# Kernel tuning notes

Hardware: AMD Instinct MI355X
Metric: run time of the kernel (lower is better)

The kernel has to match this reference:

```python
import math
import jax, jax.numpy as jnp
import numpy as np

B, T, C = 8, 4096, 1024
N_HEAD = 16
HS = C // N_HEAD  # head_size = 64


def _keep_indices(T):
    # Faithful Python/math replication of the row-gather index list.
    a = math.ceil(T / 4)
    keep = [T - 1 - x for x in range(a)]
    keep += [T - 1 - math.ceil(3 / a * (x - a) ** 2 + a) for x in range(a, math.ceil(T / 2))]
    return np.array(list(reversed(keep)), dtype=np.int32)  # [K] = [ceil(T/2)]


def setup_inputs() -> dict:
    key = jax.random.key(0)
    ks = jax.random.split(key, 7)
    s = 1.0 / math.sqrt(C)  # torch Linear default init scale
    return {
        "x": jax.random.normal(ks[0], (B, T, C), dtype=jnp.float32),
        "Wq": jax.random.uniform(ks[1], (HS, C), jnp.float32, -s, s),
        "bq": jax.random.uniform(ks[2], (HS,), jnp.float32, -s, s),
        "Wk": jax.random.uniform(ks[3], (HS, C), jnp.float32, -s, s),
        "bk": jax.random.uniform(ks[4], (HS,), jnp.float32, -s, s),
        "Wv": jax.random.uniform(ks[5], (HS, C), jnp.float32, -s, s),
        "bv": jax.random.uniform(ks[6], (HS,), jnp.float32, -s, s),
    }


def reference(x, Wq, bq, Wk, bk, Wv, bv):
    Bx, Tx, Cx = x.shape
    keep = jnp.asarray(_keep_indices(Tx))                    # [K], static
    q = x @ Wq.T + bq                                        # [B,T,hs]
    k = x @ Wk.T + bk                                        # [B,T,hs]
    v = x @ Wv.T + bv                                        # [B,T,hs]
    # Original computes full q@k^T then gathers rows; gathering q rows first
    # is the same math without materializing [B,T,T].
    qg = q[:, keep, :]                                       # [B,K,hs]
    att = jnp.einsum('bkd,btd->bkt', qg, k) * (Cx ** -0.5)   # scale by n_embd, per source
    # fade_tril = tril[keep, :T]: row i allows positions j <= keep[i]
    mask = jnp.arange(Tx)[None, :] <= keep[:, None]          # [K,T]
    att = jnp.where(mask[None], att, -jnp.inf)
    att = jax.nn.softmax(att, axis=-1)
    # dropout p=0.0 -> identity
    out = jnp.einsum('bkt,btd->bkd', att, v)                 # [B,K,hs]
    return out
```

## Files before the change

### kernel.cpp

```cpp
#include <hip/hip_runtime.h>
#include <hip/hip_bf16.h>

typedef __attribute__((ext_vector_type(8))) short s8v;
typedef __attribute__((ext_vector_type(4))) short s4v;
typedef __attribute__((ext_vector_type(4))) float f4v;

#define B_   8
#define T_   4096
#define C_   1024
#define HS_  64
#define K2_  2048

__device__ __forceinline__ int keep_of(int i) {
    if (i >= 1024) return 2048 + i;
    int d = 1023 - i;
    return 3071 - ((3 * d * d + 1023) >> 10);
}

__device__ __forceinline__ short bf16_bits(float f) {
    union { __hip_bfloat16 h; short s; } u;
    u.h = __float2bfloat16(f);
    return u.s;
}

__device__ __forceinline__ s8v cvt8f(const float* p) {
    const f4v a = *(const f4v*)p;
    const f4v b = *(const f4v*)(p + 4);
    s8v r;
    r[0] = bf16_bits(a[0]); r[1] = bf16_bits(a[1]);
    r[2] = bf16_bits(a[2]); r[3] = bf16_bits(a[3]);
    r[4] = bf16_bits(b[0]); r[5] = bf16_bits(b[1]);
    r[6] = bf16_bits(b[2]); r[7] = bf16_bits(b[3]);
    return r;
}

__device__ __forceinline__ void gload_lds16(const void* g, void* l) {
    __builtin_amdgcn_global_load_lds(
        (__attribute__((address_space(1))) void*)(g),
        (__attribute__((address_space(3))) void*)(l), 16, 0, 0);
}

__global__ __launch_bounds__(256) void wcvt_kernel(
    const float* __restrict__ Wq, const float* __restrict__ Wk,
    const float* __restrict__ Wv, short* __restrict__ Wb)
{
    const int idx = (blockIdx.x * 256 + threadIdx.x) * 8;
    const int mat = idx >> 16;
    const int off = idx & 65535;
    const float* src = (mat == 0) ? Wq : (mat == 1) ? Wk : Wv;
    *(s8v*)(Wb + idx) = cvt8f(src + off);
}

__global__ __launch_bounds__(256) void qkv_kernel(
    const float* __restrict__ x,
    const short* __restrict__ Wb,
    const float* __restrict__ bq, const float* __restrict__ bk,
    const float* __restrict__ bv,
    __hip_bfloat16* __restrict__ Qo, __hip_bfloat16* __restrict__ Ko,
    __hip_bfloat16* __restrict__ Vt)
{
    __shared__ __align__(16) char smem[40960];
    float* xs  = (float*)smem;
    short* wsm = (short*)(smem + 16384);

    const int tid  = threadIdx.x;
    const int wave = tid >> 6;
    const int lane = tid & 63;
    const int l16  = lane & 15;
    const int quad = lane >> 4;
    const int row0 = blockIdx.x * 64;

    f4v acc[3][4];
    #pragma unroll
    for (int m = 0; m < 3; ++m)
        #pragma unroll
        for (int mt = 0; mt < 4; ++mt) {
            acc[m][mt][0] = 0.f; acc[m][mt][1] = 0.f;
            acc[m][mt][2] = 0.f; acc[m][mt][3] = 0.f;
        }

    int xrow[4], xoff[4];
    #pragma unroll
    for (int i = 0; i < 4; ++i) {
        const int f = 256 * i + tid;
        xrow[i] = f >> 4;
        xoff[i] = ((f & 15) ^ (xrow[i] & 7)) * 4;
    }
    int wrow[6], woff[6];
    #pragma unroll
    for (int i = 0; i < 6; ++i) {
        const int f = 256 * i + tid;
        wrow[i] = f >> 3;
        woff[i] = ((f & 7) ^ (wrow[i] & 7)) * 8;
    }

    for (int k0 = 0; k0 < C_; k0 += 64) {
        __syncthreads();
        #pragma unroll
        for (int i = 0; i < 4; ++i)
            gload_lds16(x + (size_t)(row0 + xrow[i]) * C_ + k0 + xoff[i],
                        (char*)xs + (256 * i + tid) * 16);
        #pragma unroll
        for (int i = 0; i < 6; ++i)
            gload_lds16(Wb + (size_t)wrow[i] * C_ + k0 + woff[i],
                        (char*)wsm + (256 * i + tid) * 16);
        __syncthreads();

        #pragma unroll
        for (int kh = 0; kh < 2; ++kh) {
            s8v a[4];
            #pragma unroll
            for (int mt = 0; mt < 4; ++mt) {
                const int r   = mt * 16 + l16;
                const int ch0 = kh * 8 + quad * 2;
                const float* p0 = xs + r * 64 + ((ch0    ) ^ (r & 7)) * 4;
                const float* p1 = xs + r * 64 + ((ch0 + 1) ^ (r & 7)) * 4;
                const f4v u = *(const f4v*)p0;
                const f4v v = *(const f4v*)p1;
                s8v af;
                af[0] = bf16_bits(u[0]); af[1] = bf16_bits(u[1]);
                af[2] = bf16_bits(u[2]); af[3] = bf16_bits(u[3]);
                af[4] = bf16_bits(v[0]); af[5] = bf16_bits(v[1]);
                af[6] = bf16_bits(v[2]); af[7] = bf16_bits(v[3]);
                a[mt] = af;
            }
            #pragma unroll
            for (int m = 0; m < 3; ++m) {
                const int wr = m * 64 + wave * 16 + l16;
                const int ch = kh * 4 + quad;
                const s8v bf = *(const s8v*)(wsm + wr * 64 + ((ch ^ (wr & 7)) * 8));
                #pragma unroll
                for (int mt = 0; mt < 4; ++mt)
                    acc[m][mt] = __builtin_amdgcn_mfma_f32_16x16x32_bf16(a[mt], bf, acc[m][mt], 0, 0, 0);
            }
        }
    }

    const int wc = wave * 16 + l16;
    const float bqv = bq[wc], bkv = bk[wc], bvv = bv[wc];
    #pragma unroll
    for (int mt = 0; mt < 4; ++mt) {
        const int rbase = row0 + mt * 16 + quad * 4;
        #pragma unroll
        for (int r = 0; r < 4; ++r) {
            Qo[(size_t)(rbase + r) * HS_ + wc] = __float2bfloat16(acc[0][mt][r] + bqv);
            Ko[(size_t)(rbase + r) * HS_ + wc] = __float2bfloat16(acc[1][mt][r] + bkv);
        }
        s4v vp;
        #pragma unroll
        for (int r = 0; r < 4; ++r) vp[r] = bf16_bits(acc[2][mt][r] + bvv);
        const int bb = rbase >> 12;
        const int t  = rbase & (T_ - 1);
        *(s4v*)(Vt + (size_t)bb * HS_ * T_
                   + (size_t)(t & ~63) * HS_ + wc * 64 + (t & 63)) = vp;
    }
}

__global__ __launch_bounds__(256) void attn_kernel(
    const __hip_bfloat16* __restrict__ Qo,
    const __hip_bfloat16* __restrict__ Ko,
    const __hip_bfloat16* __restrict__ Vt,
    float* __restrict__ out)
{
    __shared__ __align__(16) char smem[73728];
    short* Ks = (short*)smem;
    short* Vs = (short*)(smem + 32768);
    float* mL = (float*)smem;
    float* mO = (float*)(smem + 256);

    const int b    = blockIdx.x & 7;
    const int pp   = blockIdx.x >> 3;
    const int tid  = threadIdx.x;
    const int wave = tid >> 6;
    const int lane = tid & 63;
    const int l16  = lane & 15;
    const int quad = lane >> 4;

    short* pw = (short*)(smem + 65536) + wave * 1024;

    const short* kb = (const short*)Ko + (size_t)b * T_ * HS_;
    const short* vb = (const short*)Vt + (size_t)b * HS_ * T_;

    int kgoff[8], vgoff[8];
    #pragma unroll
    for (int j = 0; j < 8; ++j) {
        const int ki = j * 256 + tid;
        const int kr = ki >> 3;
        kgoff[j] = kr * 64 + (((tid & 7) ^ (kr & 7)) * 8);
        const int vs_ = ki >> 9;
        const int vd  = (ki & 511) >> 3;
        vgoff[j] = (vs_ * 64 + vd) * 64 + (((tid & 7) ^ (vd & 7)) * 8);
    }

    #pragma unroll 1
    for (int which = 0; which < 2; ++which) {
        const int qb = which ? (63 - pp) : (64 + pp);

        const int qt = keep_of(qb * 16 + l16);
        const __hip_bfloat16* qrow = Qo + ((size_t)(b * T_ + qt)) * HS_;
        const s8v aq0 = *(const s8v*)(qrow + quad * 8);
        const s8v aq1 = *(const s8v*)(qrow + 32 + quad * 8);

        int keepr[4];
        #pragma unroll
        for (int r = 0; r < 4; ++r) keepr[r] = keep_of(qb * 16 + quad * 4 + r);

        const int kmin   = keep_of(qb * 16);
        const int tmax   = keep_of(qb * 16 + 15);
        const int ntiles = (tmax >> 6) + 1;
        const int nsteps = (ntiles + 3) >> 2;

        f4v accO[4];
        #pragma unroll
        for (int j = 0; j < 4; ++j) { accO[j][0]=0.f; accO[j][1]=0.f; accO[j][2]=0.f; accO[j][3]=0.f; }
        float l_p[4] = {0.f, 0.f, 0.f, 0.f};

        for (int s = 0; s < nsteps; ++s) {
            const int t064 = s << 14;

            __syncthreads();
            #pragma unroll
            for (int j = 0; j < 8; ++j)
                gload_lds16(kb + t064 + kgoff[j], (char*)smem + (j * 256 + tid) * 16);
            #pragma unroll
            for (int j = 0; j < 8; ++j)
                gload_lds16(vb + t064 + vgoff[j], (char*)smem + 32768 + (j * 256 + tid) * 16);
            __syncthreads();

            const int ttg = s * 4 + wave;
            if (ttg < ntiles) {
                const int t0 = ttg << 6;

                f4v s4[4];
                #pragma unroll
                for (int jn = 0; jn < 4; ++jn) {
                    const int row = wave * 64 + jn * 16 + l16;
                    const s8v bk0 = *(const s8v*)(Ks + row * 64 + (((quad    ) ^ (row & 7)) * 8));
                    const s8v bk1 = *(const s8v*)(Ks + row * 64 + (((quad + 4) ^ (row & 7)) * 8));
                    f4v z; z[0]=0.f; z[1]=0.f; z[2]=0.f; z[3]=0.f;
                    z = __builtin_amdgcn_mfma_f32_16x16x32_bf16(aq0, bk0, z, 0, 0, 0);
                    z = __builtin_amdgcn_mfma_f32_16x16x32_bf16(aq1, bk1, z, 0, 0, 0);
                    s4[jn] = z;
                }

                if (t0 + 63 <= kmin) {
                    #pragma unroll
                    for (int jn = 0; jn < 4; ++jn) {
                        const int t = jn * 16 + l16;
                        const int chunk = t >> 3;
                        #pragma unroll
                        for (int r = 0; r < 4; ++r) {
                            const float p = __expf(s4[jn][r] * 0.03125f);
                            l_p[r] += p;
                            const int m = quad * 4 + r;
                            pw[m * 64 + ((chunk ^ (m & 7)) * 8) + (t & 7)] = bf16_bits(p);
                        }
                    }
                } else {
                    #pragma unroll
                    for (int jn = 0; jn < 4; ++jn) {
                        const int t = jn * 16 + l16;
                        const int valid_t = t0 + t;
                        const int chunk = t >> 3;
                        #pragma unroll
                        for (int r = 0; r < 4; ++r) {
                            const float e = __expf(s4[jn][r] * 0.03125f);
                            const float p = (valid_t <= keepr[r]) ? e : 0.0f;
                            l_p[r] += p;
                            const int m = quad * 4 + r;
                            pw[m * 64 + ((chunk ^ (m & 7)) * 8) + (t & 7)] = bf16_bits(p);
                        }
                    }
                }
                const s8v ap0 = *(const s8v*)(pw + l16 * 64 + ((quad    ) ^ (l16 & 7)) * 8);
                const s8v ap1 = *(const s8v*)(pw + l16 * 64 + ((quad + 4) ^ (l16 & 7)) * 8);

                #pragma unroll
                for (int jd = 0; jd < 4; ++jd) {
                    const int rd = jd * 16 + l16;
                    const s8v bv0 = *(const s8v*)(Vs + wave * 4096 + rd * 64 + (((quad    ) ^ (rd & 7)) * 8));
                    const s8v bv1 = *(const s8v*)(Vs + wave * 4096 + rd * 64 + (((quad + 4) ^ (rd & 7)) * 8));
                    accO[jd] = __builtin_amdgcn_mfma_f32_16x16x32_bf16(ap0, bv0, accO[jd], 0, 0, 0);
                    accO[jd] = __builtin_amdgcn_mfma_f32_16x16x32_bf16(ap1, bv1, accO[jd], 0, 0, 0);
                }
            }
        }

        #pragma unroll
        for (int off = 1; off < 16; off <<= 1)
            #pragma unroll
            for (int r = 0; r < 4; ++r) l_p[r] += __shfl_xor(l_p[r], off);

        __syncthreads();
        #pragma unroll
        for (int r = 0; r < 4; ++r) {
            const int row = quad * 4 + r;
            if (l16 == 0) mL[wave * 16 + row] = l_p[r];
            #pragma unroll
            for (int jd = 0; jd < 4; ++jd)
                mO[wave * 1024 + row * 64 + jd * 16 + l16] = accO[jd][r];
        }
        __syncthreads();

        {
            const int row = tid >> 4;
            const int col = (tid & 15) * 4;
            float L = 0.f;
            #pragma unroll
            for (int w = 0; w < 4; ++w) L += mL[w * 16 + row];
            const float inv = 1.0f / L;
            f4v o; o[0]=0.f; o[1]=0.f; o[2]=0.f; o[3]=0.f;
            #pragma unroll
            for (int w = 0; w < 4; ++w) {
                const f4v ow = *(const f4v*)(mO + w * 1024 + row * 64 + col);
                #pragma unroll
                for (int j = 0; j < 4; ++j) o[j] += ow[j];
            }
            #pragma unroll
            for (int j = 0; j < 4; ++j) o[j] *= inv;
            *(f4v*)(out + ((size_t)(b * K2_ + qb * 16 + row)) * HS_ + col) = o;
        }
        __syncthreads();
    }
}

extern "C" void kernel_launch(void* const* d_in, const int* in_sizes, int n_in,
                              void* d_out, int out_size, void* d_ws, size_t ws_size,
                              hipStream_t stream) {
    (void)in_sizes; (void)n_in; (void)out_size; (void)ws_size;
    const float* x  = (const float*)d_in[0];
    const float* Wq = (const float*)d_in[1];
    const float* bq = (const float*)d_in[2];
    const float* Wk = (const float*)d_in[3];
    const float* bk = (const float*)d_in[4];
    const float* Wv = (const float*)d_in[5];
    const float* bv = (const float*)d_in[6];

    __hip_bfloat16* Qo = (__hip_bfloat16*)d_ws;
    __hip_bfloat16* Ko = Qo + (size_t)B_ * T_ * HS_;
    __hip_bfloat16* Vt = Ko + (size_t)B_ * T_ * HS_;
    short*          Wb = (short*)(Vt + (size_t)B_ * HS_ * T_);
    float* o = (float*)d_out;

    wcvt_kernel<<<dim3(96), dim3(256), 0, stream>>>(Wq, Wk, Wv, Wb);
    qkv_kernel<<<dim3((B_ * T_) / 64), dim3(256), 0, stream>>>(
        x, Wb, bq, bk, bv, Qo, Ko, Vt);
    attn_kernel<<<dim3(512), dim3(256), 0, stream>>>(Qo, Ko, Vt, o);
}
```

Before: 252.6 us.

## Double-buffer LDS tiles in QKV projection and attention with finer key chunks

The QKV projection loop now double-buffers its x and weight tiles in shared memory, so loads for the next K slice are issued before the current slice is computed. The attention kernel also double-buffers its K/V tiles and shrinks each wave's key chunk from 64 to 32 positions. That cuts per-step staging and makes the causal tail finer-grained, while the next tile's load overlaps compute. The cost is double the LDS in the QKV kernel, which may reduce occupancy, plus more loop iterations with half as many MFMAs per step in attention.

```diff
diff --git a/kernel.cpp b/kernel.cpp
--- a/kernel.cpp
+++ b/kernel.cpp
@@ -59,9 +59,7 @@
     __hip_bfloat16* __restrict__ Qo, __hip_bfloat16* __restrict__ Ko,
     __hip_bfloat16* __restrict__ Vt)
 {
-    __shared__ __align__(16) char smem[40960];
-    float* xs  = (float*)smem;
-    short* wsm = (short*)(smem + 16384);
+    __shared__ __align__(16) char smem[81920];
 
     const int tid  = threadIdx.x;
     const int wave = tid >> 6;
@@ -94,17 +92,34 @@
         woff[i] = ((f & 7) ^ (wrow[i] & 7)) * 8;
     }
 
-    for (int k0 = 0; k0 < C_; k0 += 64) {
-        __syncthreads();
-        #pragma unroll
-        for (int i = 0; i < 4; ++i)
-            gload_lds16(x + (size_t)(row0 + xrow[i]) * C_ + k0 + xoff[i],
-                        (char*)xs + (256 * i + tid) * 16);
-        #pragma unroll
-        for (int i = 0; i < 6; ++i)
-            gload_lds16(Wb + (size_t)wrow[i] * C_ + k0 + woff[i],
-                        (char*)wsm + (256 * i + tid) * 16);
-        __syncthreads();
+    #pragma unroll
+    for (int i = 0; i < 4; ++i)
+        gload_lds16(x + (size_t)(row0 + xrow[i]) * C_ + xoff[i],
+                    (char*)smem + (256 * i + tid) * 16);
+    #pragma unroll
+    for (int i = 0; i < 6; ++i)
+        gload_lds16(Wb + (size_t)wrow[i] * C_ + woff[i],
+                    (char*)smem + 32768 + (256 * i + tid) * 16);
+    __syncthreads();
+
+    int buf = 0;
+    for (int ks = 0; ks < 16; ++ks) {
+        if (ks < 15) {
+            const int k0n = (ks + 1) * 64;
+            const int xb = (buf ^ 1) * 16384;
+            const int wb2 = (buf ^ 1) * 24576;
+            #pragma unroll
+            for (int i = 0; i < 4; ++i)
+                gload_lds16(x + (size_t)(row0 + xrow[i]) * C_ + k0n + xoff[i],
+                            (char*)smem + xb + (256 * i + tid) * 16);
+            #pragma unroll
+            for (int i = 0; i < 6; ++i)
+                gload_lds16(Wb + (size_t)wrow[i] * C_ + k0n + woff[i],
+                            (char*)smem + 32768 + wb2 + (256 * i + tid) * 16);
+        }
+
+        const float* xsc = (const float*)(smem + buf * 16384);
+        const short* wsc = (const short*)(smem + 32768 + buf * 24576);
 
         #pragma unroll
         for (int kh = 0; kh < 2; ++kh) {
@@ -113,8 +128,8 @@
             for (int mt = 0; mt < 4; ++mt) {
                 const int r   = mt * 16 + l16;
                 const int ch0 = kh * 8 + quad * 2;
-                const float* p0 = xs + r * 64 + ((ch0    ) ^ (r & 7)) * 4;
-                const float* p1 = xs + r * 64 + ((ch0 + 1) ^ (r & 7)) * 4;
+                const float* p0 = xsc + r * 64 + ((ch0    ) ^ (r & 7)) * 4;
+                const float* p1 = xsc + r * 64 + ((ch0 + 1) ^ (r & 7)) * 4;
                 const f4v u = *(const f4v*)p0;
                 const f4v v = *(const f4v*)p1;
                 s8v af;
@@ -128,12 +143,14 @@
             for (int m = 0; m < 3; ++m) {
                 const int wr = m * 64 + wave * 16 + l16;
                 const int ch = kh * 4 + quad;
-                const s8v bf = *(const s8v*)(wsm + wr * 64 + ((ch ^ (wr & 7)) * 8));
+                const s8v bf = *(const s8v*)(wsc + wr * 64 + ((ch ^ (wr & 7)) * 8));
                 #pragma unroll
                 for (int mt = 0; mt < 4; ++mt)
                     acc[m][mt] = __builtin_amdgcn_mfma_f32_16x16x32_bf16(a[mt], bf, acc[m][mt], 0, 0, 0);
             }
         }
+        __syncthreads();
+        buf ^= 1;
     }
 
     const int wc = wave * 16 + l16;
@@ -162,9 +179,9 @@
     const __hip_bfloat16* __restrict__ Vt,
     float* __restrict__ out)
 {
-    __shared__ __align__(16) char smem[73728];
-    short* Ks = (short*)smem;
-    short* Vs = (short*)(smem + 32768);
+    __shared__ __align__(16) char smem[69632];
+    short* Kb = (short*)smem;
+    short* Vb = (short*)(smem + 32768);
     float* mL = (float*)smem;
     float* mO = (float*)(smem + 256);
 
@@ -176,20 +193,20 @@
     const int l16  = lane & 15;
     const int quad = lane >> 4;
 
-    short* pw = (short*)(smem + 65536) + wave * 1024;
+    short* pw = (short*)(smem + 65536) + wave * 512;
 
     const short* kb = (const short*)Ko + (size_t)b * T_ * HS_;
     const short* vb = (const short*)Vt + (size_t)b * HS_ * T_;
 
-    int kgoff[8], vgoff[8];
-    #pragma unroll
-    for (int j = 0; j < 8; ++j) {
-        const int ki = j * 256 + tid;
-        const int kr = ki >> 3;
-        kgoff[j] = kr * 64 + (((tid & 7) ^ (kr & 7)) * 8);
-        const int vs_ = ki >> 9;
-        const int vd  = (ki & 511) >> 3;
-        vgoff[j] = (vs_ * 64 + vd) * 64 + (((tid & 7) ^ (vd & 7)) * 8);
+    int koff[4], voff[4];
+    #pragma unroll
+    for (int i = 0; i < 4; ++i) {
+        const int f = i * 256 + tid;
+        const int kr = f >> 3;
+        koff[i] = kr * 64 + (((f & 7) ^ (kr & 7)) * 8);
+        const int vt_ = f >> 9;
+        const int vd  = (f >> 3) & 63;
+        voff[i] = vt_ * 4096 + vd * 64 + (((f & 7) ^ (vd & 7)) * 8);
     }
 
     #pragma unroll 1
@@ -207,83 +224,96 @@
 
         const int kmin   = keep_of(qb * 16);
         const int tmax   = keep_of(qb * 16 + 15);
-        const int ntiles = (tmax >> 6) + 1;
-        const int nsteps = (ntiles + 3) >> 2;
+        const int nt32   = (tmax >> 5) + 1;
+        const int nsteps = (nt32 + 3) >> 2;
 
         f4v accO[4];
         #pragma unroll
         for (int j = 0; j < 4; ++j) { accO[j][0]=0.f; accO[j][1]=0.f; accO[j][2]=0.f; accO[j][3]=0.f; }
         float l_p[4] = {0.f, 0.f, 0.f, 0.f};
 
+        #pragma unroll
+        for (int i = 0; i < 4; ++i)
+            gload_lds16(kb + koff[i], (char*)smem + (i * 256 + tid) * 16);
+        #pragma unroll
+        for (int i = 0; i < 4; ++i)
+            gload_lds16(vb + voff[i], (char*)smem + 32768 + (i * 256 + tid) * 16);
+        __syncthreads();
+
+        int buf = 0;
         for (int s = 0; s < nsteps; ++s) {
-            const int t064 = s << 14;
-
-            __syncthreads();
-            #pragma unroll
-            for (int j = 0; j < 8; ++j)
-                gload_lds16(kb + t064 + kgoff[j], (char*)smem + (j * 256 + tid) * 16);
-            #pragma unroll
-            for (int j = 0; j < 8; ++j)
-                gload_lds16(vb + t064 + vgoff[j], (char*)smem + 32768 + (j * 256 + tid) * 16);
-            __syncthreads();
-
-            const int ttg = s * 4 + wave;
-            if (ttg < ntiles) {
-                const int t0 = ttg << 6;
-
-                f4v s4[4];
-                #pragma unroll
-                for (int jn = 0; jn < 4; ++jn) {
-                    const int row = wave * 64 + jn * 16 + l16;
-                    const s8v bk0 = *(const s8v*)(Ks + row * 64 + (((quad    ) ^ (row & 7)) * 8));
-                    const s8v bk1 = *(const s8v*)(Ks + row * 64 + (((quad + 4) ^ (row & 7)) * 8));
+            if (s + 1 < nsteps) {
+                const int goff = (s + 1) * 8192;
+                const int ldsb = (buf ^ 1) * 16384;
+                #pragma unroll
+                for (int i = 0; i < 4; ++i)
+                    gload_lds16(kb + goff + koff[i],
+                                (char*)smem + ldsb + (i * 256 + tid) * 16);
+                #pragma unroll
+                for (int i = 0; i < 4; ++i)
+                    gload_lds16(vb + goff + voff[i],
+                                (char*)smem + 32768 + ldsb + (i * 256 + tid) * 16);
+            }
+
+            const int c = s * 4 + wave;
+            if (c < nt32) {
+                const int t0 = c << 5;
+                const short* Kc = Kb + buf * 8192;
+                const short* Vc = Vb + buf * 8192 + (wave >> 1) * 4096;
+                const int tch = (wave & 1) * 4;
+
+                f4v s2[2];
+                #pragma unroll
+                for (int jn = 0; jn < 2; ++jn) {
+                    const int row = wave * 32 + jn * 16 + l16;
+                    const s8v bk0 = *(const s8v*)(Kc + row * 64 + (((quad    ) ^ (row & 7)) * 8));
+                    const s8v bk1 = *(const s8v*)(Kc + row * 64 + (((quad + 4) ^ (row & 7)) * 8));
                     f4v z; z[0]=0.f; z[1]=0.f; z[2]=0.f; z[3]=0.f;
                     z = __builtin_amdgcn_mfma_f32_16x16x32_bf16(aq0, bk0, z, 0, 0, 0);
                     z = __builtin_amdgcn_mfma_f32_16x16x32_bf16(aq1, bk1, z, 0, 0, 0);
-                    s4[jn] = z;
+                    s2[jn] = z;
                 }
 
-                if (t0 + 63 <= kmin) {
+                if (t0 + 31 <= kmin) {
                     #pragma unroll
-                    for (int jn = 0; jn < 4; ++jn) {
+                    for (int jn = 0; jn < 2; ++jn) {
                         const int t = jn * 16 + l16;
                         const int chunk = t >> 3;
                         #pragma unroll
                         for (int r = 0; r < 4; ++r) {
-                            const float p = __expf(s4[jn][r] * 0.03125f);
+                            const float p = __expf(s2[jn][r] * 0.03125f);
                             l_p[r] += p;
                             const int m = quad * 4 + r;
-                            pw[m * 64 + ((chunk ^ (m & 7)) * 8) + (t & 7)] = bf16_bits(p);
+                            pw[m * 32 + ((chunk ^ (m & 3)) * 8) + (t & 7)] = bf16_bits(p);
                         }
                     }
                 } else {
                     #pragma unroll
-                    for (int jn = 0; jn < 4; ++jn) {
+                    for (int jn = 0; jn < 2; ++jn) {
                         const int t = jn * 16 + l16;
                         const int valid_t = t0 + t;
                         const int chunk = t >> 3;
                         #pragma unroll
                         for (int r = 0; r < 4; ++r) {
-                            const float e = __expf(s4[jn][r] * 0.03125f);
+                            const float e = __expf(s2[jn][r] * 0.03125f);
                             const float p = (valid_t <= keepr[r]) ? e : 0.0f;
                             l_p[r] += p;
                             const int m = quad * 4 + r;
-                            pw[m * 64 + ((chunk ^ (m & 7)) * 8) + (t & 7)] = bf16_bits(p);
+                            pw[m * 32 + ((chunk ^ (m & 3)) * 8) + (t & 7)] = bf16_bits(p);
                         }
                     }
                 }
-                const s8v ap0 = *(const s8v*)(pw + l16 * 64 + ((quad    ) ^ (l16 & 7)) * 8);
-                const s8v ap1 = *(const s8v*)(pw + l16 * 64 + ((quad + 4) ^ (l16 & 7)) * 8);
+                const s8v ap = *(const s8v*)(pw + l16 * 32 + ((quad ^ (l16 & 3)) * 8));
 
                 #pragma unroll
                 for (int jd = 0; jd < 4; ++jd) {
                     const int rd = jd * 16 + l16;
-                    const s8v bv0 = *(const s8v*)(Vs + wave * 4096 + rd * 64 + (((quad    ) ^ (rd & 7)) * 8));
-                    const s8v bv1 = *(const s8v*)(Vs + wave * 4096 + rd * 64 + (((quad + 4) ^ (rd & 7)) * 8));
-                    accO[jd] = __builtin_amdgcn_mfma_f32_16x16x32_bf16(ap0, bv0, accO[jd], 0, 0, 0);
-                    accO[jd] = __builtin_amdgcn_mfma_f32_16x16x32_bf16(ap1, bv1, accO[jd], 0, 0, 0);
+                    const s8v bv = *(const s8v*)(Vc + rd * 64 + (((tch + quad) ^ (rd & 7)) * 8));
+                    accO[jd] = __builtin_amdgcn_mfma_f32_16x16x32_bf16(ap, bv, accO[jd], 0, 0, 0);
                 }
             }
+            __syncthreads();
+            buf ^= 1;
         }
 
         #pragma unroll
```

Result: slower. 260.5 us (+3.1%).

## Process both query blocks in one pass over shared K/V tiles

Applied to the files above, without the earlier changes.

Each block used to stream its K/V tiles twice, once for each of its two paired query blocks. Now both query blocks are processed against the same staged K/V tile in a single loop, and the K and V fragments are loaded from LDS into registers once and reused. Block-to-work mapping is also reversed so the heaviest blocks launch first. This halves the global-to-LDS loads and barriers but roughly doubles accumulator register pressure, which may lower occupancy.

```diff
diff --git a/kernel.cpp b/kernel.cpp
--- a/kernel.cpp
+++ b/kernel.cpp
@@ -169,7 +169,7 @@
     float* mO = (float*)(smem + 256);
 
     const int b    = blockIdx.x & 7;
-    const int pp   = blockIdx.x >> 3;
+    const int pp   = 63 - (blockIdx.x >> 3);
     const int tid  = threadIdx.x;
     const int wave = tid >> 6;
     const int lane = tid & 63;
@@ -192,58 +192,75 @@
         vgoff[j] = (vs_ * 64 + vd) * 64 + (((tid & 7) ^ (vd & 7)) * 8);
     }
 
-    #pragma unroll 1
-    for (int which = 0; which < 2; ++which) {
-        const int qb = which ? (63 - pp) : (64 + pp);
-
+    const int qbs[2] = { 64 + pp, 63 - pp };
+
+    s8v aq[2][2];
+    int keepr[2][4], kmin[2], ntl[2];
+    #pragma unroll
+    for (int e = 0; e < 2; ++e) {
+        const int qb = qbs[e];
         const int qt = keep_of(qb * 16 + l16);
         const __hip_bfloat16* qrow = Qo + ((size_t)(b * T_ + qt)) * HS_;
-        const s8v aq0 = *(const s8v*)(qrow + quad * 8);
-        const s8v aq1 = *(const s8v*)(qrow + 32 + quad * 8);
-
-        int keepr[4];
-        #pragma unroll
-        for (int r = 0; r < 4; ++r) keepr[r] = keep_of(qb * 16 + quad * 4 + r);
-
-        const int kmin   = keep_of(qb * 16);
-        const int tmax   = keep_of(qb * 16 + 15);
-        const int ntiles = (tmax >> 6) + 1;
-        const int nsteps = (ntiles + 3) >> 2;
-
-        f4v accO[4];
-        #pragma unroll
-        for (int j = 0; j < 4; ++j) { accO[j][0]=0.f; accO[j][1]=0.f; accO[j][2]=0.f; accO[j][3]=0.f; }
-        float l_p[4] = {0.f, 0.f, 0.f, 0.f};
-
-        for (int s = 0; s < nsteps; ++s) {
-            const int t064 = s << 14;
-
-            __syncthreads();
-            #pragma unroll
-            for (int j = 0; j < 8; ++j)
-                gload_lds16(kb + t064 + kgoff[j], (char*)smem + (j * 256 + tid) * 16);
-            #pragma unroll
-            for (int j = 0; j < 8; ++j)
-                gload_lds16(vb + t064 + vgoff[j], (char*)smem + 32768 + (j * 256 + tid) * 16);
-            __syncthreads();
-
-            const int ttg = s * 4 + wave;
-            if (ttg < ntiles) {
-                const int t0 = ttg << 6;
+        aq[e][0] = *(const s8v*)(qrow + quad * 8);
+        aq[e][1] = *(const s8v*)(qrow + 32 + quad * 8);
+        #pragma unroll
+        for (int r = 0; r < 4; ++r) keepr[e][r] = keep_of(qb * 16 + quad * 4 + r);
+        kmin[e] = keep_of(qb * 16);
+        ntl[e]  = (keep_of(qb * 16 + 15) >> 6) + 1;
+    }
+    const int nsteps = (ntl[0] + 3) >> 2;
+
+    f4v accO[2][4];
+    float l_p[2][4];
+    #pragma unroll
+    for (int e = 0; e < 2; ++e)
+        #pragma unroll
+        for (int j = 0; j < 4; ++j) {
+            accO[e][j][0]=0.f; accO[e][j][1]=0.f; accO[e][j][2]=0.f; accO[e][j][3]=0.f;
+            l_p[e][j] = 0.f;
+        }
+
+    for (int s = 0; s < nsteps; ++s) {
+        const int t064 = s << 14;
+
+        __syncthreads();
+        #pragma unroll
+        for (int j = 0; j < 8; ++j)
+            gload_lds16(kb + t064 + kgoff[j], (char*)smem + (j * 256 + tid) * 16);
+        #pragma unroll
+        for (int j = 0; j < 8; ++j)
+            gload_lds16(vb + t064 + vgoff[j], (char*)smem + 32768 + (j * 256 + tid) * 16);
+        __syncthreads();
+
+        const int ttg = s * 4 + wave;
+        if (ttg < ntl[0]) {
+            const int t0 = ttg << 6;
+
+            s8v bk0[4], bk1[4], bv0[4], bv1[4];
+            #pragma unroll
+            for (int j = 0; j < 4; ++j) {
+                const int row = wave * 64 + j * 16 + l16;
+                bk0[j] = *(const s8v*)(Ks + row * 64 + (((quad    ) ^ (row & 7)) * 8));
+                bk1[j] = *(const s8v*)(Ks + row * 64 + (((quad + 4) ^ (row & 7)) * 8));
+                const int rd = j * 16 + l16;
+                bv0[j] = *(const s8v*)(Vs + wave * 4096 + rd * 64 + (((quad    ) ^ (rd & 7)) * 8));
+                bv1[j] = *(const s8v*)(Vs + wave * 4096 + rd * 64 + (((quad + 4) ^ (rd & 7)) * 8));
+            }
+
+            #pragma unroll
+            for (int e = 0; e < 2; ++e) {
+                if (e == 1 && ttg >= ntl[1]) break;
 
                 f4v s4[4];
                 #pragma unroll
                 for (int jn = 0; jn < 4; ++jn) {
-                    const int row = wave * 64 + jn * 16 + l16;
-                    const s8v bk0 = *(const s8v*)(Ks + row * 64 + (((quad    ) ^ (row & 7)) * 8));
-                    const s8v bk1 = *(const s8v*)(Ks + row * 64 + (((quad + 4) ^ (row & 7)) * 8));
                     f4v z; z[0]=0.f; z[1]=0.f; z[2]=0.f; z[3]=0.f;
-                    z = __builtin_amdgcn_mfma_f32_16x16x32_bf16(aq0, bk0, z, 0, 0, 0);
-                    z = __builtin_amdgcn_mfma_f32_16x16x32_bf16(aq1, bk1, z, 0, 0, 0);
+                    z = __builtin_amdgcn_mfma_f32_16x16x32_bf16(aq[e][0], bk0[jn], z, 0, 0, 0);
+                    z = __builtin_amdgcn_mfma_f32_16x16x32_bf16(aq[e][1], bk1[jn], z, 0, 0, 0);
                     s4[jn] = z;
                 }
 
-                if (t0 + 63 <= kmin) {
+                if (t0 + 63 <= kmin[e]) {
                     #pragma unroll
                     for (int jn = 0; jn < 4; ++jn) {
                         const int t = jn * 16 + l16;
@@ -251,7 +268,7 @@
                         #pragma unroll
                         for (int r = 0; r < 4; ++r) {
                             const float p = __expf(s4[jn][r] * 0.03125f);
-                            l_p[r] += p;
+                            l_p[e][r] += p;
                             const int m = quad * 4 + r;
                             pw[m * 64 + ((chunk ^ (m & 7)) * 8) + (t & 7)] = bf16_bits(p);
                         }
@@ -264,9 +281,9 @@
                         const int chunk = t >> 3;
                         #pragma unroll
                         for (int r = 0; r < 4; ++r) {
-                            const float e = __expf(s4[jn][r] * 0.03125f);
-                            const float p = (valid_t <= keepr[r]) ? e : 0.0f;
-                            l_p[r] += p;
+                            const float ex = __expf(s4[jn][r] * 0.03125f);
+                            const float p = (valid_t <= keepr[e][r]) ? ex : 0.0f;
+                            l_p[e][r] += p;
                             const int m = quad * 4 + r;
                             pw[m * 64 + ((chunk ^ (m & 7)) * 8) + (t & 7)] = bf16_bits(p);
                         }
@@ -277,28 +294,29 @@
 
                 #pragma unroll
                 for (int jd = 0; jd < 4; ++jd) {
-                    const int rd = jd * 16 + l16;
-                    const s8v bv0 = *(const s8v*)(Vs + wave * 4096 + rd * 64 + (((quad    ) ^ (rd & 7)) * 8));
-                    const s8v bv1 = *(const s8v*)(Vs + wave * 4096 + rd * 64 + (((quad + 4) ^ (rd & 7)) * 8));
-                    accO[jd] = __builtin_amdgcn_mfma_f32_16x16x32_bf16(ap0, bv0, accO[jd], 0, 0, 0);
-                    accO[jd] = __builtin_amdgcn_mfma_f32_16x16x32_bf16(ap1, bv1, accO[jd], 0, 0, 0);
+                    accO[e][jd] = __builtin_amdgcn_mfma_f32_16x16x32_bf16(ap0, bv0[jd], accO[e][jd], 0, 0, 0);
+                    accO[e][jd] = __builtin_amdgcn_mfma_f32_16x16x32_bf16(ap1, bv1[jd], accO[e][jd], 0, 0, 0);
                 }
             }
         }
-
+    }
+
+    #pragma unroll 1
+    for (int e = 0; e < 2; ++e) {
+        const int qb = qbs[e];
         #pragma unroll
         for (int off = 1; off < 16; off <<= 1)
             #pragma unroll
-            for (int r = 0; r < 4; ++r) l_p[r] += __shfl_xor(l_p[r], off);
+            for (int r = 0; r < 4; ++r) l_p[e][r] += __shfl_xor(l_p[e][r], off);
 
         __syncthreads();
         #pragma unroll
         for (int r = 0; r < 4; ++r) {
             const int row = quad * 4 + r;
-            if (l16 == 0) mL[wave * 16 + row] = l_p[r];
+            if (l16 == 0) mL[wave * 16 + row] = l_p[e][r];
             #pragma unroll
             for (int jd = 0; jd < 4; ++jd)
-                mO[wave * 1024 + row * 64 + jd * 16 + l16] = accO[jd][r];
+                mO[wave * 1024 + row * 64 + jd * 16 + l16] = accO[e][jd][r];
         }
         __syncthreads();
 
@@ -320,7 +338,6 @@
             for (int j = 0; j < 4; ++j) o[j] *= inv;
             *(f4v*)(out + ((size_t)(b * K2_ + qb * 16 + row)) * HS_ + col) = o;
         }
-        __syncthreads();
     }
 }
 
```

Measured after the change: 283.9 us. 12.4% more time.
